# Performance work log

Measured on AMD Instinct MI355X. Metric: run time of the kernel, lower is better.

The kernel has to match this reference:

```python
import jax, jax.numpy as jnp
import numpy as np
from jax import lax

VOCAB = 1000
TMAX = 1001  # max_episode_length + 1
L = 2048
H_GRU = 256


def setup_inputs() -> dict:
    key = jax.random.key(0)
    ks = jax.random.split(key, 40)
    g = lambda i, shape, s: jax.random.normal(ks[i], shape, dtype=jnp.float32) * s
    inp = {
        "x": jax.random.normal(ks[0], (1, 3, 124, 124), dtype=jnp.float32),
        "curr_instr": jax.random.randint(ks[1], (1, L), 0, VOCAB),
        "prev_instr": jax.random.randint(ks[2], (1, L), 0, VOCAB),
        "next_instr": jax.random.randint(ks[3], (1, L), 0, VOCAB),
        "tx": jax.random.randint(ks[4], (1,), 0, TMAX),
        "hx": jnp.zeros((1, 768), jnp.float32),
        "cx": jnp.zeros((1, 768), jnp.float32),
        # conv stack
        "conv1_w": g(5, (128, 3, 8, 8), 0.05), "conv1_b": jnp.zeros((128,), jnp.float32),
        "conv2_w": g(6, (64, 128, 4, 4), 0.03), "conv2_b": jnp.zeros((64,), jnp.float32),
        "conv3_w": g(7, (64, 64, 4, 4), 0.03), "conv3_b": jnp.zeros((64,), jnp.float32),
        # embeddings
        "emb": g(8, (VOCAB, 32), 0.1),
        "time_emb": g(9, (TMAX, 32), 0.1),
        # GRU (torch nn.GRU layout: 3*H rows for r,z,n)
        "gru_w_ih": g(10, (3 * H_GRU, 32), 0.1), "gru_w_hh": g(11, (3 * H_GRU, H_GRU), 0.06),
        "gru_b_ih": jnp.zeros((3 * H_GRU,), jnp.float32), "gru_b_hh": jnp.zeros((3 * H_GRU,), jnp.float32),
        # attention linear 256 -> 64
        "attn_w": g(12, (64, H_GRU), 0.06), "attn_b": jnp.zeros((64,), jnp.float32),
        # image-fusion linear 64*6*6 -> 256
        "lin_w": g(13, (256, 64 * 6 * 6), 0.02), "lin_b": jnp.zeros((256,), jnp.float32),
        # LSTMCell 768 -> 768 (torch layout: 4*H rows for i,f,g,o)
        "lstm_w_ih": g(14, (4 * 768, 768), 0.03), "lstm_w_hh": g(15, (4 * 768, 768), 0.03),
        "lstm_b_ih": jnp.zeros((4 * 768,), jnp.float32), "lstm_b_hh": jnp.zeros((4 * 768,), jnp.float32),
        # heads over [hx, time_emb] = 768 + 32 = 800
        "critic_w": g(16, (1, 800), 0.03), "critic_b": jnp.zeros((1,), jnp.float32),
        "actor_w": g(17, (4, 800), 0.01), "actor_b": jnp.zeros((4,), jnp.float32),
    }
    return inp


def _conv(x, w, b, s):
    return lax.conv_general_dilated(x, w, (s, s), "VALID") + b[None, :, None, None]


def reference(x, curr_instr, prev_instr, next_instr, tx, hx, cx,
              conv1_w, conv1_b, conv2_w, conv2_b, conv3_w, conv3_b,
              emb, time_emb, gru_w_ih, gru_w_hh, gru_b_ih, gru_b_hh,
              attn_w, attn_b, lin_w, lin_b,
              lstm_w_ih, lstm_w_hh, lstm_b_ih, lstm_b_hh,
              critic_w, critic_b, actor_w, actor_b):
    # image tower: [1,3,124,124] -> [1,64,6,6]
    h1 = jax.nn.relu(_conv(x, conv1_w, conv1_b, 4))
    h2 = jax.nn.relu(_conv(h1, conv2_w, conv2_b, 2))
    x_image_rep = jax.nn.relu(_conv(h2, conv3_w, conv3_b, 2))

    # three instruction sequences, encoded by a shared GRU (vmapped scan)
    tokens = jnp.stack([curr_instr[0], prev_instr[0], next_instr[0]])  # [3, L]

    def gru_encode(tok):
        xs = emb[tok]                               # [L, 32]
        gi_all = xs @ gru_w_ih.T + gru_b_ih         # precompute input gates [L, 3H]
        def step(h, gi):
            gh = h @ gru_w_hh.T + gru_b_hh
            i_r, i_z, i_n = jnp.split(gi, 3)
            h_r, h_z, h_n = jnp.split(gh, 3)
            r = jax.nn.sigmoid(i_r + h_r)
            z = jax.nn.sigmoid(i_z + h_z)
            n = jnp.tanh(i_n + r * h_n)
            return (1.0 - z) * n + z * h, None
        h, _ = lax.scan(step, jnp.zeros((H_GRU,), xs.dtype), gi_all)
        return h

    h3 = jax.vmap(gru_encode)(tokens)               # [3, 256]
    attn = jax.nn.sigmoid(h3 @ attn_w.T + attn_b)   # [3, 64]

    # BUG-FAITHFUL: original forward uses cached_computation['curr_x_attention']
    # for all three branches, so the three fused features are identical.
    curr_attn = attn[0][None, :, None, None]        # [1,64,1,1]
    fused = (x_image_rep * curr_attn).reshape(1, -1)  # [1, 2304]
    feat = jax.nn.relu(fused @ lin_w.T + lin_b)     # [1, 256]
    xcat = jnp.concatenate([feat, feat, feat], axis=1)  # [1, 768]

    # LSTMCell
    gates = xcat @ lstm_w_ih.T + lstm_b_ih + hx @ lstm_w_hh.T + lstm_b_hh  # [1, 3072]
    gi, gf, gg, go = jnp.split(gates, 4, axis=1)
    cx_new = jax.nn.sigmoid(gf) * cx + jax.nn.sigmoid(gi) * jnp.tanh(gg)
    hx_new = jax.nn.sigmoid(go) * jnp.tanh(cx_new)

    t = time_emb[tx].reshape(-1, 32)                # [1, 32]
    z = jnp.concatenate([hx_new, t], axis=1)        # [1, 800]
    critic = z @ critic_w.T + critic_b              # [1, 1]
    actor = z @ actor_w.T + actor_b                 # [1, 4]
    return critic, actor, hx_new, cx_new
```

## Files before the change

kernel.cpp:

```cpp
#include <hip/hip_runtime.h>
#include <hip/hip_bf16.h>
#include <stdint.h>


typedef _Float16 half8 __attribute__((ext_vector_type(8)));
typedef _Float16 half2v __attribute__((ext_vector_type(2)));
typedef float f32x4 __attribute__((ext_vector_type(4)));

__device__ __forceinline__ float sigm(float x) { return 1.0f / (1.0f + __expf(-x)); }
__device__ __forceinline__ float tanh_f(float x) { return 2.0f / (1.0f + __expf(-2.0f * x)) - 1.0f; }

__global__ void k_pack(const float* __restrict__ whh, uint32_t* __restrict__ wf16p) {
    int i = blockIdx.x * 256 + threadIdx.x;
    if (i >= 98304) return;
    half2v p = {(_Float16)whh[2 * i], (_Float16)whh[2 * i + 1]};
    wf16p[i] = __builtin_bit_cast(uint32_t, p);
}

__global__ void k_conv1(const float* __restrict__ x, const float* __restrict__ w,
                        const float* __restrict__ b, float* __restrict__ h1) {
    int idx = blockIdx.x * 256 + threadIdx.x;
    if (idx >= 128 * 30 * 30) return;
    int ox = idx % 30, oy = (idx / 30) % 30, oc = idx / 900;
    const float* wr = w + oc * 192;
    float acc = b[oc];
    for (int c = 0; c < 3; ++c)
        for (int ky = 0; ky < 8; ++ky) {
            const float* xr = x + (c * 124 + oy * 4 + ky) * 124 + ox * 4;
            const float* wk = wr + (c * 8 + ky) * 8;
#pragma unroll
            for (int kx = 0; kx < 8; ++kx) acc = fmaf(xr[kx], wk[kx], acc);
        }
    h1[idx] = fmaxf(acc, 0.0f);
}

__global__ void k_conv2(const float* __restrict__ h1, const float* __restrict__ w,
                        const float* __restrict__ b, float* __restrict__ h2) {
    int idx = blockIdx.x * 256 + threadIdx.x;
    if (idx >= 64 * 14 * 14) return;
    int ox = idx % 14, oy = (idx / 14) % 14, oc = idx / 196;
    float acc = b[oc];
    const float* wr = w + oc * 128 * 16;
    for (int c = 0; c < 128; ++c) {
#pragma unroll
        for (int ky = 0; ky < 4; ++ky) {
            const float* hr = h1 + (c * 30 + oy * 2 + ky) * 30 + ox * 2;
            const float* wk = wr + (c * 4 + ky) * 4;
#pragma unroll
            for (int kx = 0; kx < 4; ++kx) acc = fmaf(hr[kx], wk[kx], acc);
        }
    }
    h2[idx] = fmaxf(acc, 0.0f);
}

__global__ void k_conv3(const float* __restrict__ h2, const float* __restrict__ w,
                        const float* __restrict__ b, float* __restrict__ x3) {
    int idx = blockIdx.x * 256 + threadIdx.x;
    if (idx >= 64 * 6 * 6) return;
    int ox = idx % 6, oy = (idx / 6) % 6, oc = idx / 36;
    float acc = b[oc];
    const float* wr = w + oc * 64 * 16;
    for (int c = 0; c < 64; ++c) {
#pragma unroll
        for (int ky = 0; ky < 4; ++ky) {
            const float* hr = h2 + (c * 14 + oy * 2 + ky) * 14 + ox * 2;
            const float* wk = wr + (c * 4 + ky) * 4;
#pragma unroll
            for (int kx = 0; kx < 4; ++kx) acc = fmaf(hr[kx], wk[kx], acc);
        }
    }
    x3[idx] = fmaxf(acc, 0.0f);
}

__global__ void k_gi(const int* __restrict__ curr, const float* __restrict__ emb,
                     const float* __restrict__ wih, const float* __restrict__ bih,
                     const float* __restrict__ bhh, float* __restrict__ gi) {
    int idx = blockIdx.x * 256 + threadIdx.x;
    int j = idx % 768, t = idx / 768;
    int tok = curr[t];
    const float4* e = (const float4*)(emb + tok * 32);
    const float4* wr = (const float4*)(wih + j * 32);
    float acc = bih[j] + (j < 512 ? bhh[j] : 0.0f);
#pragma unroll
    for (int k = 0; k < 8; ++k) {
        float4 ev = e[k], wv = wr[k];
        acc = fmaf(ev.x, wv.x, acc);
        acc = fmaf(ev.y, wv.y, acc);
        acc = fmaf(ev.z, wv.z, acc);
        acc = fmaf(ev.w, wv.w, acc);
    }
    gi[idx] = acc;
}

#define FOR8(X, nt) X(nt, 0) X(nt, 1) X(nt, 2) X(nt, 3) X(nt, 4) X(nt, 5) X(nt, 6) X(nt, 7)
#define FOR6(Y) Y(0) Y(1) Y(2) Y(3) Y(4) Y(5)

#define DECLB(nt, kt) uint4 b##nt##_##kt;
#define DECLBROW(nt) FOR8(DECLB, nt)
#define LOADB(nt, kt) b##nt##_##kt = wp##nt[kt * 4 + quad];
#define LOADBROW(nt) \
    { const uint4* wp##nt = wb4 + (size_t)(TB##nt + n16) * 32; FOR8(LOADB, nt) }
#define TIEB(nt, kt) \
    asm volatile("" : "+v"(b##nt##_##kt.x), "+v"(b##nt##_##kt.y), "+v"(b##nt##_##kt.z), "+v"(b##nt##_##kt.w));
#define TIEBROW(nt) FOR8(TIEB, nt)
#define DECLACC(nt) f32x4 acc##nt;
#define ZEROACC(nt) acc##nt = (f32x4)(0.0f);
#define MF(nt, kt) \
    acc##nt = __builtin_amdgcn_mfma_f32_16x16x32_f16(a##kt, __builtin_bit_cast(half8, b##nt##_##kt), acc##nt, 0, 0, 0);
#define MFK(kt) MF(0, kt) MF(2, kt) MF(4, kt) MF(1, kt) MF(3, kt) MF(5, kt)
#define LOADA(kt) half8 a##kt = __builtin_bit_cast(half8, abase[kt * 4 + quad]);

#define SC 0.0009765625f

#define GRU_BODY(PIN, POUT)                                                       \
    {                                                                             \
        float gvR0 = 0.f, gvZ0 = 0.f, gvN0 = 0.f;                                 \
        float gvR1 = 0.f, gvZ1 = 0.f, gvN1 = 0.f;                                 \
        if (lane < 16) {                                                          \
            gvR0 = gp[0];  gvZ0 = gp[256]; gvN0 = gp[512];                        \
            gvR1 = gp[16]; gvZ1 = gp[272]; gvN1 = gp[528];                        \
        }                                                                         \
        gp += 768;                                                                \
        const uint4* abase = (n16 == 1) ? (const uint4*)hbuf[PIN][1]              \
                                        : (const uint4*)hbuf[PIN][0];             \
        FOR6(ZEROACC)                                                             \
        LOADA(0) LOADA(1)                                                         \
        MFK(0)                                                                    \
        LOADA(2)                                                                  \
        MFK(1)                                                                    \
        LOADA(3)                                                                  \
        MFK(2)                                                                    \
        LOADA(4)                                                                  \
        MFK(3)                                                                    \
        LOADA(5)                                                                  \
        MFK(4)                                                                    \
        LOADA(6)                                                                  \
        MFK(5)                                                                    \
        LOADA(7)                                                                  \
        MFK(6)                                                                    \
        MFK(7)                                                                    \
        if (lane < 16) {                                                          \
            float yR0 = fmaf(acc0.y, SC, acc0.x) + gvR0;                          \
            float yZ0 = fmaf(acc2.y, SC, acc2.x) + gvZ0;                          \
            float yN0 = fmaf(acc4.y, SC, acc4.x) + bN0;                           \
            float r0 = sigm(yR0), z0 = sigm(yZ0);                                 \
            float n0 = tanh_f(fmaf(r0, yN0, gvN0));                               \
            h0 = fmaf(z0, h0 - n0, n0);                                           \
            float yR1 = fmaf(acc1.y, SC, acc1.x) + gvR1;                          \
            float yZ1 = fmaf(acc3.y, SC, acc3.x) + gvZ1;                          \
            float yN1 = fmaf(acc5.y, SC, acc5.x) + bN1;                           \
            float r1 = sigm(yR1), z1 = sigm(yZ1);                                 \
            float n1 = tanh_f(fmaf(r1, yN1, gvN1));                               \
            h1 = fmaf(z1, h1 - n1, n1);                                           \
            _Float16 hi0 = (_Float16)h0, hi1 = (_Float16)h1;                      \
            hbuf[POUT][0][e0] = hi0;                                              \
            hbuf[POUT][1][e0] = (_Float16)((h0 - (float)hi0) * 1024.0f);          \
            hbuf[POUT][0][e1] = hi1;                                              \
            hbuf[POUT][1][e1] = (_Float16)((h1 - (float)hi1) * 1024.0f);          \
        }                                                                         \
        __syncthreads();                                                          \
    }

__global__ __attribute__((amdgpu_flat_work_group_size(512, 512), amdgpu_waves_per_eu(2, 2)))
void k_gru_scan(const float* __restrict__ gi, const uint32_t* __restrict__ wf16p,
                const float* __restrict__ bhh, const float* __restrict__ attn_w,
                const float* __restrict__ attn_b, float* __restrict__ attn0) {
    __shared__ __align__(16) _Float16 hbuf[2][2][256];
    const int tid = threadIdx.x;
    const int lane = tid & 63;
    const int wv = tid >> 6;
    const int n16 = lane & 15;
    const int quad = lane >> 4;

    const int TB0 = 32 * wv, TB1 = TB0 + 16;
    const int TB2 = 256 + TB0, TB3 = 256 + TB1;
    const int TB4 = 512 + TB0, TB5 = 512 + TB1;
    const int e0 = TB0 + n16, e1 = TB1 + n16;

    FOR6(DECLBROW)
    {
        const uint4* wb4 = (const uint4*)wf16p;
        FOR6(LOADBROW)
    }
    FOR6(TIEBROW)
    FOR6(DECLACC)

    const float bN0 = bhh[512 + e0];
    const float bN1 = bhh[512 + e1];

    float h0 = 0.0f, h1 = 0.0f;
    if (tid < 256) {
        hbuf[0][0][tid] = (_Float16)0.0f;
        hbuf[0][1][tid] = (_Float16)0.0f;
    }
    __syncthreads();

    const float* gp = gi + e0;

#pragma clang loop unroll(disable)
    for (int it = 0; it < 1024; ++it) {
        GRU_BODY(0, 1)
        GRU_BODY(1, 0)
    }

    if (tid < 64) {
        const float* ar = attn_w + tid * 256;
        float acc = attn_b[tid];
        for (int k = 0; k < 256; ++k) {
            float hk = (float)hbuf[0][0][k] + (float)hbuf[0][1][k] * SC;
            acc = fmaf(ar[k], hk, acc);
        }
        attn0[tid] = sigm(acc);
    }
}

__global__ void k_feat(const float* __restrict__ x3, const float* __restrict__ attn0,
                       const float* __restrict__ lw, const float* __restrict__ lb,
                       float* __restrict__ feat) {
    __shared__ __align__(16) float fused[2304];
    int t = threadIdx.x;
    for (int i = t; i < 2304; i += 64) fused[i] = x3[i] * attn0[i / 36];
    __syncthreads();
    int row = blockIdx.x * 64 + t;
    const float4* wvv = (const float4*)(lw + (size_t)row * 2304);
    float acc = lb[row];
    for (int i = 0; i < 576; ++i) {
        float4 v = wvv[i];
        const float* f = fused + i * 4;
        acc = fmaf(v.x, f[0], acc);
        acc = fmaf(v.y, f[1], acc);
        acc = fmaf(v.z, f[2], acc);
        acc = fmaf(v.w, f[3], acc);
    }
    feat[row] = fmaxf(acc, 0.0f);
}

__global__ void k_lstm_gates(const float* __restrict__ wih, const float* __restrict__ whh,
                             const float* __restrict__ bih, const float* __restrict__ bhh,
                             const float* __restrict__ hx, const float* __restrict__ feat,
                             float* __restrict__ gates) {
    int wid = threadIdx.x >> 6, lane = threadIdx.x & 63;
    int row = blockIdx.x * 4 + wid;
    const float* wi = wih + (size_t)row * 768;
    const float* wh = whh + (size_t)row * 768;
    float acc = 0.0f;
#pragma unroll
    for (int i = 0; i < 12; ++i) {
        int k = lane + i * 64;
        acc = fmaf(wi[k], feat[k & 255], acc);
        acc = fmaf(wh[k], hx[k], acc);
    }
#pragma unroll
    for (int s = 32; s; s >>= 1) acc += __shfl_down(acc, s, 64);
    if (lane == 0) gates[row] = acc + bih[row] + bhh[row];
}

__global__ void k_lstm_cell(const float* __restrict__ gates, const float* __restrict__ cx,
                            float* __restrict__ out, float* __restrict__ hxf) {
    int i = threadIdx.x;
    float g_i = gates[i], g_f = gates[768 + i], g_g = gates[1536 + i], g_o = gates[2304 + i];
    float c = cx[i];
    float cn = sigm(g_f) * c + sigm(g_i) * tanh_f(g_g);
    float hn = sigm(g_o) * tanh_f(cn);
    out[5 + i] = hn;
    out[5 + 768 + i] = cn;
    hxf[i] = hn;
}

__global__ void k_heads(const float* __restrict__ hxf, const float* __restrict__ temb,
                        const int* __restrict__ tx, const float* __restrict__ cw,
                        const float* __restrict__ cb, const float* __restrict__ aw,
                        const float* __restrict__ ab, float* __restrict__ out) {
    __shared__ float z[800];
    int t = threadIdx.x;
    for (int i = t; i < 768; i += 320) z[i] = hxf[i];
    if (t < 32) z[768 + t] = temb[tx[0] * 32 + t];
    __syncthreads();
    int w = t >> 6, lane = t & 63;
    const float* row = (w == 0) ? cw : (aw + (size_t)(w - 1) * 800);
    float acc = 0.0f;
    for (int k = lane; k < 800; k += 64) acc = fmaf(row[k], z[k], acc);
#pragma unroll
    for (int s = 32; s; s >>= 1) acc += __shfl_down(acc, s, 64);
    if (lane == 0) {
        float b = (w == 0) ? cb[0] : ab[w - 1];
        out[w] = acc + b;
    }
}

extern "C" void kernel_launch(void* const* d_in, const int* in_sizes, int n_in,
                              void* d_out, int out_size, void* d_ws, size_t ws_size,
                              hipStream_t stream) {
    const float* x = (const float*)d_in[0];
    const int* curr = (const int*)d_in[1];
    const int* tx = (const int*)d_in[4];
    const float* hx = (const float*)d_in[5];
    const float* cx = (const float*)d_in[6];
    const float* c1w = (const float*)d_in[7];
    const float* c1b = (const float*)d_in[8];
    const float* c2w = (const float*)d_in[9];
    const float* c2b = (const float*)d_in[10];
    const float* c3w = (const float*)d_in[11];
    const float* c3b = (const float*)d_in[12];
    const float* emb = (const float*)d_in[13];
    const float* temb = (const float*)d_in[14];
    const float* gwih = (const float*)d_in[15];
    const float* gwhh = (const float*)d_in[16];
    const float* gbih = (const float*)d_in[17];
    const float* gbhh = (const float*)d_in[18];
    const float* attw = (const float*)d_in[19];
    const float* attb = (const float*)d_in[20];
    const float* linw = (const float*)d_in[21];
    const float* linb = (const float*)d_in[22];
    const float* lwih = (const float*)d_in[23];
    const float* lwhh = (const float*)d_in[24];
    const float* lbih = (const float*)d_in[25];
    const float* lbhh = (const float*)d_in[26];
    const float* cw = (const float*)d_in[27];
    const float* cb = (const float*)d_in[28];
    const float* aw = (const float*)d_in[29];
    const float* ab = (const float*)d_in[30];
    float* out = (float*)d_out;

    char* ws = (char*)d_ws;
    float* gi = (float*)(ws + 0);
    float* h1 = (float*)(ws + 6291456);
    float* h2 = (float*)(ws + 6752256);
    float* x3 = (float*)(ws + 6802432);
    float* attn0 = (float*)(ws + 6811648);
    float* feat = (float*)(ws + 6811904);
    float* gates = (float*)(ws + 6812928);
    float* hxf = (float*)(ws + 6825216);
    uint32_t* wf16p = (uint32_t*)(ws + 6828288);

    k_pack<<<384, 256, 0, stream>>>(gwhh, wf16p);
    k_gi<<<6144, 256, 0, stream>>>(curr, emb, gwih, gbih, gbhh, gi);
    k_conv1<<<450, 256, 0, stream>>>(x, c1w, c1b, h1);
    k_conv2<<<49, 256, 0, stream>>>(h1, c2w, c2b, h2);
    k_conv3<<<9, 256, 0, stream>>>(h2, c3w, c3b, x3);
    k_gru_scan<<<1, 512, 0, stream>>>(gi, wf16p, gbhh, attw, attb, attn0);
    k_feat<<<4, 64, 0, stream>>>(x3, attn0, linw, linb, feat);
    k_lstm_gates<<<768, 256, 0, stream>>>(lwih, lwhh, lbih, lbhh, hx, feat, gates);
    k_lstm_cell<<<1, 768, 0, stream>>>(gates, cx, out, hxf);
    k_heads<<<1, 320, 0, stream>>>(hxf, temb, tx, cw, cb, aw, ab, out);
}
```

Before: 2.625 ms.

## Rotate GRU K-chunks per wave and start own-slice MFMAs before barrier

Each wave now walks the K dimension starting from its own 32-element slice of the hidden state, rotated by wave index. The MFMAs for that slice are issued right after the wave writes its new h, before the barrier, so part of the next step's matmul overlaps synchronisation. Rotating start offsets also spreads LDS reads across banks between waves. s_setprio raises wave priority during the MFMA chain. The cost is more intricate scheduling and an explicit lgkmcnt wait, which relies on the wave reading only the values its own lanes wrote before the barrier.

```diff
diff --git a/kernel.cpp b/kernel.cpp
--- a/kernel.cpp
+++ b/kernel.cpp
@@ -95,20 +95,22 @@
 #define FOR8(X, nt) X(nt, 0) X(nt, 1) X(nt, 2) X(nt, 3) X(nt, 4) X(nt, 5) X(nt, 6) X(nt, 7)
 #define FOR6(Y) Y(0) Y(1) Y(2) Y(3) Y(4) Y(5)
 
-#define DECLB(nt, kt) uint4 b##nt##_##kt;
+#define DECLB(nt, s) uint4 b##nt##_##s;
 #define DECLBROW(nt) FOR8(DECLB, nt)
-#define LOADB(nt, kt) b##nt##_##kt = wp##nt[kt * 4 + quad];
+#define LOADB(nt, s) b##nt##_##s = wp##nt[off##s];
 #define LOADBROW(nt) \
     { const uint4* wp##nt = wb4 + (size_t)(TB##nt + n16) * 32; FOR8(LOADB, nt) }
-#define TIEB(nt, kt) \
-    asm volatile("" : "+v"(b##nt##_##kt.x), "+v"(b##nt##_##kt.y), "+v"(b##nt##_##kt.z), "+v"(b##nt##_##kt.w));
+#define TIEB(nt, s) \
+    asm volatile("" : "+v"(b##nt##_##s.x), "+v"(b##nt##_##s.y), "+v"(b##nt##_##s.z), "+v"(b##nt##_##s.w));
 #define TIEBROW(nt) FOR8(TIEB, nt)
 #define DECLACC(nt) f32x4 acc##nt;
 #define ZEROACC(nt) acc##nt = (f32x4)(0.0f);
-#define MF(nt, kt) \
-    acc##nt = __builtin_amdgcn_mfma_f32_16x16x32_f16(a##kt, __builtin_bit_cast(half8, b##nt##_##kt), acc##nt, 0, 0, 0);
-#define MFK(kt) MF(0, kt) MF(2, kt) MF(4, kt) MF(1, kt) MF(3, kt) MF(5, kt)
-#define LOADA(kt) half8 a##kt = __builtin_bit_cast(half8, abase[kt * 4 + quad]);
+#define MF(nt, s) \
+    acc##nt = __builtin_amdgcn_mfma_f32_16x16x32_f16(a##s, __builtin_bit_cast(half8, b##nt##_##s), acc##nt, 0, 0, 0);
+#define MF0(nt) \
+    acc##nt = __builtin_amdgcn_mfma_f32_16x16x32_f16(aown, __builtin_bit_cast(half8, b##nt##_0), zero4, 0, 0, 0);
+#define MFK(s) MF(0, s) MF(4, s) MF(2, s) MF(1, s) MF(5, s) MF(3, s)
+#define LOADA(s) half8 a##s = __builtin_bit_cast(half8, abIN[off##s]);
 
 #define SC 0.0009765625f
 
@@ -121,12 +123,9 @@
             gvR1 = gp[16]; gvZ1 = gp[272]; gvN1 = gp[528];                        \
         }                                                                         \
         gp += 768;                                                                \
-        const uint4* abase = (n16 == 1) ? (const uint4*)hbuf[PIN][1]              \
-                                        : (const uint4*)hbuf[PIN][0];             \
-        FOR6(ZEROACC)                                                             \
-        LOADA(0) LOADA(1)                                                         \
-        MFK(0)                                                                    \
-        LOADA(2)                                                                  \
+        const uint4* abIN = hb##PIN;                                              \
+        __builtin_amdgcn_s_setprio(1);                                            \
+        LOADA(1) LOADA(2)                                                         \
         MFK(1)                                                                    \
         LOADA(3)                                                                  \
         MFK(2)                                                                    \
@@ -139,6 +138,7 @@
         LOADA(7)                                                                  \
         MFK(6)                                                                    \
         MFK(7)                                                                    \
+        __builtin_amdgcn_s_setprio(0);                                            \
         if (lane < 16) {                                                          \
             float yR0 = fmaf(acc0.y, SC, acc0.x) + gvR0;                          \
             float yZ0 = fmaf(acc2.y, SC, acc2.x) + gvZ0;                          \
@@ -158,6 +158,11 @@
             hbuf[POUT][0][e1] = hi1;                                              \
             hbuf[POUT][1][e1] = (_Float16)((h1 - (float)hi1) * 1024.0f);          \
         }                                                                         \
+        asm volatile("s_waitcnt lgkmcnt(0)" ::: "memory");                        \
+        {                                                                         \
+            half8 aown = __builtin_bit_cast(half8, hb##POUT[off0]);               \
+            MF0(0) MF0(4) MF0(2) MF0(1) MF0(5) MF0(3)                             \
+        }                                                                         \
         __syncthreads();                                                          \
     }
 
@@ -177,6 +182,15 @@
     const int TB4 = 512 + TB0, TB5 = 512 + TB1;
     const int e0 = TB0 + n16, e1 = TB1 + n16;
 
+    const int off0 = ((wv + 0) & 7) * 4 + quad;
+    const int off1 = ((wv + 1) & 7) * 4 + quad;
+    const int off2 = ((wv + 2) & 7) * 4 + quad;
+    const int off3 = ((wv + 3) & 7) * 4 + quad;
+    const int off4 = ((wv + 4) & 7) * 4 + quad;
+    const int off5 = ((wv + 5) & 7) * 4 + quad;
+    const int off6 = ((wv + 6) & 7) * 4 + quad;
+    const int off7 = ((wv + 7) & 7) * 4 + quad;
+
     FOR6(DECLBROW)
     {
         const uint4* wb4 = (const uint4*)wf16p;
@@ -184,6 +198,7 @@
     }
     FOR6(TIEBROW)
     FOR6(DECLACC)
+    const f32x4 zero4 = (f32x4)(0.0f);
 
     const float bN0 = bhh[512 + e0];
     const float bN1 = bhh[512 + e1];
@@ -193,6 +208,10 @@
         hbuf[0][0][tid] = (_Float16)0.0f;
         hbuf[0][1][tid] = (_Float16)0.0f;
     }
+    const uint4* hb0 = (const uint4*)((n16 == 1) ? hbuf[0][1] : hbuf[0][0]);
+    const uint4* hb1 = (const uint4*)((n16 == 1) ? hbuf[1][1] : hbuf[1][0]);
+
+    FOR6(ZEROACC)
     __syncthreads();
 
     const float* gp = gi + e0;
```

After: 3.003 ms. +14.4%, slower.
